# Kernel tuning notes

Hardware: AMD Instinct MI355X
Metric: run time of the kernel (lower is better)

## Reference

```python
import math
import jax, jax.numpy as jnp
import numpy as np

NUM_BUCKETS = 32
MAX_DISTANCE = 128
N_HEADS = 16
D_KV = 64


def _relative_position_bucket(relative_position, num_buckets=NUM_BUCKETS, max_distance=MAX_DISTANCE):
    # bidirectional (encoder) version, faithful to T5Attention._relative_position_bucket
    nb = num_buckets // 2
    rel_buckets = (relative_position > 0).astype(jnp.int32) * nb
    rp = jnp.abs(relative_position)
    max_exact = nb // 2
    is_small = rp < max_exact
    # log-spaced buckets for large distances; clamp arg of log to >=1 to avoid -inf
    rp_large = max_exact + (
        jnp.log(jnp.maximum(rp, 1).astype(jnp.float32) / max_exact)
        / math.log(max_distance / max_exact)
        * (nb - max_exact)
    ).astype(jnp.int32)
    rp_large = jnp.minimum(rp_large, nb - 1)
    return rel_buckets + jnp.where(is_small, rp, rp_large)


def setup_inputs() -> dict:
    key = jax.random.key(0)
    ks = jax.random.split(key, 6)
    B, S, D = 2, 2048, 1024
    scale = 0.02
    return {
        "hidden_states": jax.random.normal(ks[0], (B, S, D), dtype=jnp.float32),
        "Wq": jax.random.normal(ks[1], (D, N_HEADS * D_KV), dtype=jnp.float32) * scale,
        "Wk": jax.random.normal(ks[2], (D, N_HEADS * D_KV), dtype=jnp.float32) * scale,
        "Wv": jax.random.normal(ks[3], (D, N_HEADS * D_KV), dtype=jnp.float32) * scale,
        "Wo": jax.random.normal(ks[4], (N_HEADS * D_KV, D), dtype=jnp.float32) * scale,
        "rel_bias": jax.random.normal(ks[5], (NUM_BUCKETS, N_HEADS), dtype=jnp.float32),
    }


def reference(hidden_states, Wq, Wk, Wv, Wo, rel_bias):
    B, S, D = hidden_states.shape
    H, dk = N_HEADS, D_KV
    q = (hidden_states @ Wq).reshape(B, S, H, dk)
    k = (hidden_states @ Wk).reshape(B, S, H, dk)
    v = (hidden_states @ Wv).reshape(B, S, H, dk)

    pos = jnp.arange(S)
    relative_position = pos[None, :] - pos[:, None]          # [S_q, S_k]
    buckets = _relative_position_bucket(relative_position)    # [S_q, S_k]
    bias = rel_bias[buckets].transpose(2, 0, 1)               # [H, S_q, S_k]

    # T5 attention: NO 1/sqrt(d) scaling
    scores = jnp.einsum('bqhd,bkhd->bhqk', q, k) + bias[None]
    attn = jax.nn.softmax(scores, axis=-1)
    ctx = jnp.einsum('bhqk,bkhd->bqhd', attn, v).reshape(B, S, H * dk)
    return ctx @ Wo
```

## Files before the change

kernel.cpp:

```cpp
#include <hip/hip_runtime.h>
#include <stdint.h>

#define S_LEN 2048
#define NH 16
#define NB_DELTA (2*S_LEN-1)
#define FST 72

typedef __attribute__((ext_vector_type(8))) __bf16 bf16x8;
typedef __attribute__((ext_vector_type(4))) float f32x4;

__device__ __forceinline__ unsigned short f2bf(float f){
    union { float f; unsigned int u; } v; v.f = f;
    unsigned int u = v.u;
    return (unsigned short)((u + 0x7FFFu + ((u >> 16) & 1u)) >> 16);
}
__device__ __forceinline__ unsigned short f2bf_fast(float f){
    union { float f; unsigned int u; } v; v.f = f;
    return (unsigned short)((v.u + 0x8000u) >> 16);
}

__device__ __forceinline__ void gload16(const void* g, void* l){
    __builtin_amdgcn_global_load_lds(
        (const __attribute__((address_space(1))) void*)(uintptr_t)g,
        (__attribute__((address_space(3))) void*)(uintptr_t)l, 16, 0, 0);
}

__global__ __launch_bounds__(256) void cast_bias_kernel(const float* __restrict__ in,
                                                        unsigned short* __restrict__ out, int n,
                                                        const float* __restrict__ rel_bias,
                                                        float* __restrict__ biasT){
    int i = (blockIdx.x * blockDim.x + threadIdx.x) * 4;
    if (i < n) {
        float4 f = *(const float4*)(in + i);
        ushort4 o;
        o.x = f2bf(f.x); o.y = f2bf(f.y); o.z = f2bf(f.z); o.w = f2bf(f.w);
        *(ushort4*)(out + i) = o;
    }
    if (blockIdx.x < 16) {
        int t = blockIdx.x * 256 + threadIdx.x;
        if (t < NB_DELTA) {
            int delta = t - (S_LEN - 1);
            int bucket = (delta > 0) ? 16 : 0;
            int a = delta < 0 ? -delta : delta;
            int b;
            if (a < 8) b = a;
            else {
                int bl = 33 - __builtin_clz(a * a);
                b = bl < 15 ? bl : 15;
            }
            bucket += b;
            for (int h = 0; h < NH; h++)
                biasT[h * NB_DELTA + t] = rel_bias[bucket * NH + h];
        }
    }
}

__global__ __launch_bounds__(256) void transpose_cast4_kernel(
    const float* __restrict__ W0, const float* __restrict__ W1,
    const float* __restrict__ W2, const float* __restrict__ W3,
    unsigned short* __restrict__ D0, unsigned short* __restrict__ D1,
    unsigned short* __restrict__ D2, unsigned short* __restrict__ D3){
    const float* src; unsigned short* dst;
    switch (blockIdx.z) {
        case 0: src = W0; dst = D0; break;
        case 1: src = W1; dst = D1; break;
        case 2: src = W2; dst = D2; break;
        default: src = W3; dst = D3; break;
    }
    __shared__ float tile[32][33];
    int bx = blockIdx.x, by = blockIdx.y;
    int tx = threadIdx.x & 31, ty = threadIdx.x >> 5;
    for (int i = 0; i < 4; i++)
        tile[ty + 8*i][tx] = src[(size_t)(by*32 + ty + 8*i) * 1024 + bx*32 + tx];
    __syncthreads();
    for (int i = 0; i < 4; i++)
        dst[(size_t)(bx*32 + ty + 8*i) * 1024 + by*32 + tx] = f2bf(tile[tx][ty + 8*i]);
}

template<int MODE, int BM>
__global__ __launch_bounds__(256) void gemm_bt_kernel(const unsigned short* __restrict__ A,
                                                      const unsigned short* __restrict__ BT,
                                                      float* __restrict__ C0,
                                                      unsigned short* __restrict__ C1,
                                                      unsigned short* __restrict__ C2,
                                                      int Kdim, int ldc){
    constexpr int IT = BM / 32;
    __shared__ __align__(16) unsigned short As[BM * 32];
    __shared__ __align__(16) unsigned short Bs[128 * 32];
    const int t = threadIdx.x;
    const int wave = t >> 6, lane = t & 63;
    const int quad = lane >> 4, l16 = lane & 15;
    const int wm = (wave >> 1) * (BM / 2), wn = (wave & 1) * 64;
    const size_t row0 = (size_t)blockIdx.y * BM, col0 = (size_t)blockIdx.x * 128;

    const unsigned short* ga = A  + (row0 + wave * (BM/4) + (lane >> 2)) * (size_t)Kdim + (lane & 3) * 8;
    const unsigned short* gb = BT + (col0 + wave * 32 + (lane >> 2)) * (size_t)Kdim + (lane & 3) * 8;
    unsigned short* la0 = &As[(wave * (BM/4)) * 32];
    unsigned short* la1 = &As[(wave * (BM/4) + 16) * 32];
    unsigned short* lb0 = &Bs[(wave * 32) * 32];
    unsigned short* lb1 = &Bs[(wave * 32 + 16) * 32];
    const size_t rstep = (size_t)16 * Kdim;

    f32x4 acc[IT][4] = {};

    for (int kt = 0; kt < Kdim; kt += 32) {
        gload16(ga + kt, la0);
        if (BM == 128) gload16(ga + rstep + kt, la1);
        gload16(gb + kt,         lb0);
        gload16(gb + rstep + kt, lb1);
        __syncthreads();
        bf16x8 a[IT], b[4];
        for (int i = 0; i < IT; i++)
            a[i] = *(const bf16x8*)(&As[(wm + i*16 + l16) * 32 + quad * 8]);
        for (int j = 0; j < 4; j++)
            b[j] = *(const bf16x8*)(&Bs[(wn + j*16 + l16) * 32 + quad * 8]);
        for (int i = 0; i < IT; i++)
            for (int j = 0; j < 4; j++)
                acc[i][j] = __builtin_amdgcn_mfma_f32_16x16x32_bf16(a[i], b[j], acc[i][j], 0, 0, 0);
        __syncthreads();
    }
    for (int i = 0; i < IT; i++)
        for (int j = 0; j < 4; j++) {
            size_t r0 = row0 + wm + i*16 + quad*4;
            size_t c  = col0 + wn + j*16 + l16;
            if (MODE == 0) {
                for (int r = 0; r < 4; r++)
                    C0[(r0 + r) * ldc + c] = acc[i][j][r];
            } else {
                if (c < 2048) {
                    for (int r = 0; r < 4; r++)
                        C1[(r0 + r) * 2048 + c] = f2bf(acc[i][j][r]);
                } else {
                    int bb = (int)(r0 >> 11);
                    int s  = (int)(r0 & 2047);
                    ushort4 pk;
                    pk.x = f2bf(acc[i][j][0]); pk.y = f2bf(acc[i][j][1]);
                    pk.z = f2bf(acc[i][j][2]); pk.w = f2bf(acc[i][j][3]);
                    *(ushort4*)(C2 + ((size_t)(bb * 1024) + (c - 2048)) * 2048 + s) = pk;
                }
            }
        }
}

__global__ __launch_bounds__(256, 4) void flash5_kernel(
    const unsigned short* __restrict__ qk,
    const unsigned short* __restrict__ vt,
    const float* __restrict__ biasT,
    float* __restrict__ ctxp,
    float* __restrict__ rsbuf)
{
    const int qt = blockIdx.x, h = blockIdx.y;
    const int b = blockIdx.z >> 1, ck = blockIdx.z & 1;
    const int kt0 = ck << 10;
    const int t = threadIdx.x;
    const int w = t >> 6, lane = t & 63, quad = lane >> 4, l16 = lane & 15;
    const int q0 = qt * 128;

    __shared__ __align__(16) unsigned short smem[128 * FST];
    __shared__ __align__(16) unsigned short Pb[128 * FST];
    __shared__ float bias_s[192];
    unsigned short* Qs  = smem;
    unsigned short* Ks  = smem;
    unsigned short* Vts = smem + 64 * FST;

    for (int s = 0; s < 4; s++) {
        int g = t + s * 256;
        int r = g >> 3, c = (g & 7) * 8;
        *(int4*)&Qs[r * FST + c] =
            *(const int4*)(qk + (size_t)(b * S_LEN + q0 + r) * 2048 + h * 64 + c);
    }
    __syncthreads();
    bf16x8 qb[2][2];
    for (int nt = 0; nt < 2; nt++)
        for (int ks = 0; ks < 2; ks++)
            qb[ks][nt] = *(const bf16x8*)&Qs[(w * 32 + nt * 16 + l16) * FST + ks * 32 + quad * 8];

    float rsum[2] = {0.f, 0.f};
    f32x4 ctx[4][2] = {};

    const float* biasRow = biasT + h * NB_DELTA + 2047;

    for (int kt = kt0; kt < kt0 + 1024; kt += 64) {
        __syncthreads();
        {
            int r0 = t >> 3, c0 = (t & 7) * 8;
            int g1 = t + 256;
            int r1 = g1 >> 3, c1 = (g1 & 7) * 8;
            const unsigned short* kbase = qk + (size_t)(b * S_LEN + kt) * 2048 + 1024 + h * 64;
            *(int4*)&Ks[r0 * FST + c0] = *(const int4*)(kbase + (size_t)r0 * 2048 + c0);
            *(int4*)&Ks[r1 * FST + c1] = *(const int4*)(kbase + (size_t)r1 * 2048 + c1);
            const unsigned short* vbase = vt + (size_t)(b * 1024 + h * 64) * 2048 + kt;
            *(int4*)&Vts[r0 * FST + c0] = *(const int4*)(vbase + (size_t)r0 * 2048 + c0);
            *(int4*)&Vts[r1 * FST + c1] = *(const int4*)(vbase + (size_t)r1 * 2048 + c1);
            if (t < 192) bias_s[t] = biasRow[kt - q0 - 127 + t] - 16.0f;
        }
        __syncthreads();

        f32x4 st[4][2] = {};
        for (int ks = 0; ks < 2; ks++)
            for (int nb = 0; nb < 4; nb++) {
                bf16x8 ka = *(const bf16x8*)&Ks[(nb * 16 + l16) * FST + ks * 32 + quad * 8];
                st[nb][0] = __builtin_amdgcn_mfma_f32_16x16x32_bf16(ka, qb[ks][0], st[nb][0], 0, 0, 0);
                st[nb][1] = __builtin_amdgcn_mfma_f32_16x16x32_bf16(ka, qb[ks][1], st[nb][1], 0, 0, 0);
            }
        for (int nt = 0; nt < 2; nt++) {
            const int ib = quad * 4 + 127 - w * 32 - nt * 16 - l16;
            float rs = 0.f;
            for (int nb = 0; nb < 4; nb++) {
                float e0 = __expf(st[nb][nt][0] + bias_s[ib + nb * 16 + 0]);
                float e1 = __expf(st[nb][nt][1] + bias_s[ib + nb * 16 + 1]);
                float e2 = __expf(st[nb][nt][2] + bias_s[ib + nb * 16 + 2]);
                float e3 = __expf(st[nb][nt][3] + bias_s[ib + nb * 16 + 3]);
                rs += (e0 + e1) + (e2 + e3);
                ushort4 pk;
                pk.x = f2bf_fast(e0); pk.y = f2bf_fast(e1);
                pk.z = f2bf_fast(e2); pk.w = f2bf_fast(e3);
                *(ushort4*)&Pb[(w * 32 + nt * 16 + l16) * FST + nb * 16 + quad * 4] = pk;
            }
            rsum[nt] += rs;
        }
        for (int ks = 0; ks < 2; ks++) {
            bf16x8 pb0 = *(const bf16x8*)&Pb[(w * 32 + l16) * FST + ks * 32 + quad * 8];
            bf16x8 pb1 = *(const bf16x8*)&Pb[(w * 32 + 16 + l16) * FST + ks * 32 + quad * 8];
            for (int nd = 0; nd < 4; nd++) {
                bf16x8 va = *(const bf16x8*)&Vts[(nd * 16 + l16) * FST + ks * 32 + quad * 8];
                ctx[nd][0] = __builtin_amdgcn_mfma_f32_16x16x32_bf16(va, pb0, ctx[nd][0], 0, 0, 0);
                ctx[nd][1] = __builtin_amdgcn_mfma_f32_16x16x32_bf16(va, pb1, ctx[nd][1], 0, 0, 0);
            }
        }
    }
    float* cp = ctxp + (size_t)ck * 4096 * 1024;
    for (int nt = 0; nt < 2; nt++) {
        float rs = rsum[nt];
        rs += __shfl_xor(rs, 16, 64);
        rs += __shfl_xor(rs, 32, 64);
        int row = b * S_LEN + q0 + w * 32 + nt * 16 + l16;
        if (quad == 0) rsbuf[((size_t)ck * 4096 + row) * 16 + h] = rs;
        for (int nd = 0; nd < 4; nd++) {
            float4 pv;
            pv.x = ctx[nd][nt][0]; pv.y = ctx[nd][nt][1];
            pv.z = ctx[nd][nt][2]; pv.w = ctx[nd][nt][3];
            *(float4*)&cp[(size_t)row * 1024 + h * 64 + nd * 16 + quad * 4] = pv;
        }
    }
}

__global__ __launch_bounds__(256) void combine_kernel(const float* __restrict__ ctxp,
                                                      const float* __restrict__ rsbuf,
                                                      unsigned short* __restrict__ ctxb){
    int e = blockIdx.x * 256 + threadIdx.x;
    int row = e >> 8;
    int c4 = (e & 255) * 4;
    int h = c4 >> 6;
    float l = rsbuf[(size_t)row * 16 + h] + rsbuf[((size_t)4096 + row) * 16 + h];
    float4 a = *(const float4*)&ctxp[(size_t)row * 1024 + c4];
    float4 bb = *(const float4*)&ctxp[(size_t)4096 * 1024 + (size_t)row * 1024 + c4];
    float inv = 1.f / l;
    ushort4 o;
    o.x = f2bf((a.x + bb.x) * inv); o.y = f2bf((a.y + bb.y) * inv);
    o.z = f2bf((a.z + bb.z) * inv); o.w = f2bf((a.w + bb.w) * inv);
    *(ushort4*)&ctxb[(size_t)row * 1024 + c4] = o;
}

extern "C" void kernel_launch(void* const* d_in, const int* in_sizes, int n_in,
                              void* d_out, int out_size, void* d_ws, size_t ws_size,
                              hipStream_t stream) {
    const float* hs       = (const float*)d_in[0];
    const float* Wq       = (const float*)d_in[1];
    const float* Wk       = (const float*)d_in[2];
    const float* Wv       = (const float*)d_in[3];
    const float* Wo       = (const float*)d_in[4];
    const float* rel_bias = (const float*)d_in[5];
    float* out = (float*)d_out;

    char* ws = (char*)d_ws;
    float* biasT          = (float*)ws;           ws += 262144;
    unsigned short* hsb   = (unsigned short*)ws;  ws += 8388608;
    unsigned short* WT    = (unsigned short*)ws;  ws += 6291456;
    unsigned short* WoT   = (unsigned short*)ws;  ws += 2097152;
    unsigned short* qkbuf = (unsigned short*)ws;  ws += 16777216;
    unsigned short* Vtg   = (unsigned short*)ws;  ws += 8388608;
    unsigned short* ctxb  = (unsigned short*)ws;  ws += 8388608;
    float* ctxp           = (float*)ws;           ws += 33554432;
    float* rsbuf          = (float*)ws;

    cast_bias_kernel<<<4096, 256, 0, stream>>>(hs, hsb, 4194304, rel_bias, biasT);
    transpose_cast4_kernel<<<dim3(32, 32, 4), 256, 0, stream>>>(
        Wq, Wk, Wv, Wo, WT, WT + 1024 * 1024, WT + 2 * 1024 * 1024, WoT);

    gemm_bt_kernel<1, 128><<<dim3(24, 32), 256, 0, stream>>>(hsb, WT, nullptr, qkbuf, Vtg, 1024, 0);
    flash5_kernel<<<dim3(S_LEN / 128, NH, 4), 256, 0, stream>>>(qkbuf, Vtg, biasT, ctxp, rsbuf);
    combine_kernel<<<4096, 256, 0, stream>>>(ctxp, rsbuf, ctxb);
    gemm_bt_kernel<0, 64><<<dim3(8, 64), 256, 0, stream>>>(ctxb, WoT, out, nullptr, nullptr, 1024, 1024);
}
```

Baseline: 211.6 us.

## Merge prep kernels, use direct global-to-LDS loads, store bf16 partial context

Merges the hidden-state cast/bias kernel and the weight transpose kernel into one launch, removing one kernel launch. In the attention kernel, K/V tiles are now loaded with global_load_lds 16-byte direct copies into an unpadded split layout, bypassing registers. The per-split partial context is written as bf16 instead of fp32, halving that intermediate's write and read traffic in flash and combine. Risks are LDS bank conflicts from the unpadded 32-wide layout and extra rounding of unnormalised partial sums.

New measurement: 209.0 us. About the same (-1.3%).

```diff
diff --git a/kernel.cpp b/kernel.cpp
--- a/kernel.cpp
+++ b/kernel.cpp
@@ -4,7 +4,7 @@
 #define S_LEN 2048
 #define NH 16
 #define NB_DELTA (2*S_LEN-1)
-#define FST 72
+#define PST 72
 
 typedef __attribute__((ext_vector_type(8))) __bf16 bf16x8;
 typedef __attribute__((ext_vector_type(4))) float f32x4;
@@ -18,6 +18,10 @@
     union { float f; unsigned int u; } v; v.f = f;
     return (unsigned short)((v.u + 0x8000u) >> 16);
 }
+__device__ __forceinline__ float bf2f(unsigned short u){
+    union { unsigned int u; float f; } v; v.u = ((unsigned int)u) << 16;
+    return v.f;
+}
 
 __device__ __forceinline__ void gload16(const void* g, void* l){
     __builtin_amdgcn_global_load_lds(
@@ -25,41 +29,41 @@
         (__attribute__((address_space(3))) void*)(uintptr_t)l, 16, 0, 0);
 }
 
-__global__ __launch_bounds__(256) void cast_bias_kernel(const float* __restrict__ in,
-                                                        unsigned short* __restrict__ out, int n,
-                                                        const float* __restrict__ rel_bias,
-                                                        float* __restrict__ biasT){
-    int i = (blockIdx.x * blockDim.x + threadIdx.x) * 4;
-    if (i < n) {
-        float4 f = *(const float4*)(in + i);
-        ushort4 o;
-        o.x = f2bf(f.x); o.y = f2bf(f.y); o.z = f2bf(f.z); o.w = f2bf(f.w);
-        *(ushort4*)(out + i) = o;
-    }
-    if (blockIdx.x < 16) {
-        int t = blockIdx.x * 256 + threadIdx.x;
-        if (t < NB_DELTA) {
-            int delta = t - (S_LEN - 1);
-            int bucket = (delta > 0) ? 16 : 0;
-            int a = delta < 0 ? -delta : delta;
-            int b;
-            if (a < 8) b = a;
-            else {
-                int bl = 33 - __builtin_clz(a * a);
-                b = bl < 15 ? bl : 15;
-            }
-            bucket += b;
-            for (int h = 0; h < NH; h++)
-                biasT[h * NB_DELTA + t] = rel_bias[bucket * NH + h];
-        }
-    }
-}
-
-__global__ __launch_bounds__(256) void transpose_cast4_kernel(
+__global__ __launch_bounds__(256) void prep_kernel(
+    const float* __restrict__ hs, unsigned short* __restrict__ hsb,
     const float* __restrict__ W0, const float* __restrict__ W1,
     const float* __restrict__ W2, const float* __restrict__ W3,
     unsigned short* __restrict__ D0, unsigned short* __restrict__ D1,
-    unsigned short* __restrict__ D2, unsigned short* __restrict__ D3){
+    unsigned short* __restrict__ D2, unsigned short* __restrict__ D3,
+    const float* __restrict__ rel_bias, float* __restrict__ biasT){
+    if (blockIdx.z == 4) {
+        int bi = blockIdx.y * 32 + blockIdx.x;
+        for (int it = 0; it < 4; it++) {
+            int i = bi * 4096 + it * 1024 + threadIdx.x * 4;
+            float4 f = *(const float4*)(hs + i);
+            ushort4 o;
+            o.x = f2bf(f.x); o.y = f2bf(f.y); o.z = f2bf(f.z); o.w = f2bf(f.w);
+            *(ushort4*)(hsb + i) = o;
+        }
+        if (bi < 16) {
+            int t = bi * 256 + threadIdx.x;
+            if (t < NB_DELTA) {
+                int delta = t - (S_LEN - 1);
+                int bucket = (delta > 0) ? 16 : 0;
+                int a = delta < 0 ? -delta : delta;
+                int b;
+                if (a < 8) b = a;
+                else {
+                    int bl = 33 - __builtin_clz(a * a);
+                    b = bl < 15 ? bl : 15;
+                }
+                bucket += b;
+                for (int h = 0; h < NH; h++)
+                    biasT[h * NB_DELTA + t] = rel_bias[bucket * NH + h];
+            }
+        }
+        return;
+    }
     const float* src; unsigned short* dst;
     switch (blockIdx.z) {
         case 0: src = W0; dst = D0; break;
@@ -142,11 +146,11 @@
         }
 }
 
-__global__ __launch_bounds__(256, 4) void flash5_kernel(
+__global__ __launch_bounds__(256, 4) void flash6_kernel(
     const unsigned short* __restrict__ qk,
     const unsigned short* __restrict__ vt,
     const float* __restrict__ biasT,
-    float* __restrict__ ctxp,
+    unsigned short* __restrict__ ctxpb,
     float* __restrict__ rsbuf)
 {
     const int qt = blockIdx.x, h = blockIdx.y;
@@ -156,42 +160,43 @@
     const int w = t >> 6, lane = t & 63, quad = lane >> 4, l16 = lane & 15;
     const int q0 = qt * 128;
 
-    __shared__ __align__(16) unsigned short smem[128 * FST];
-    __shared__ __align__(16) unsigned short Pb[128 * FST];
+    __shared__ __align__(16) unsigned short KV[4][64 * 32];
+    __shared__ __align__(16) unsigned short Pb[128 * PST];
     __shared__ float bias_s[192];
-    unsigned short* Qs  = smem;
-    unsigned short* Ks  = smem;
-    unsigned short* Vts = smem + 64 * FST;
 
     for (int s = 0; s < 4; s++) {
         int g = t + s * 256;
         int r = g >> 3, c = (g & 7) * 8;
-        *(int4*)&Qs[r * FST + c] =
+        *(int4*)&Pb[r * PST + c] =
             *(const int4*)(qk + (size_t)(b * S_LEN + q0 + r) * 2048 + h * 64 + c);
     }
     __syncthreads();
     bf16x8 qb[2][2];
     for (int nt = 0; nt < 2; nt++)
         for (int ks = 0; ks < 2; ks++)
-            qb[ks][nt] = *(const bf16x8*)&Qs[(w * 32 + nt * 16 + l16) * FST + ks * 32 + quad * 8];
+            qb[ks][nt] = *(const bf16x8*)&Pb[(w * 32 + nt * 16 + l16) * PST + ks * 32 + quad * 8];
 
     float rsum[2] = {0.f, 0.f};
     f32x4 ctx[4][2] = {};
 
     const float* biasRow = biasT + h * NB_DELTA + 2047;
+
+    const int srow = w * 16 + (lane >> 2);
+    const int scol = (lane & 3) * 8;
+    unsigned short* ldsK0 = &KV[0][w * 16 * 32];
+    unsigned short* ldsK1 = &KV[1][w * 16 * 32];
+    unsigned short* ldsV0 = &KV[2][w * 16 * 32];
+    unsigned short* ldsV1 = &KV[3][w * 16 * 32];
 
     for (int kt = kt0; kt < kt0 + 1024; kt += 64) {
         __syncthreads();
         {
-            int r0 = t >> 3, c0 = (t & 7) * 8;
-            int g1 = t + 256;
-            int r1 = g1 >> 3, c1 = (g1 & 7) * 8;
-            const unsigned short* kbase = qk + (size_t)(b * S_LEN + kt) * 2048 + 1024 + h * 64;
-            *(int4*)&Ks[r0 * FST + c0] = *(const int4*)(kbase + (size_t)r0 * 2048 + c0);
-            *(int4*)&Ks[r1 * FST + c1] = *(const int4*)(kbase + (size_t)r1 * 2048 + c1);
-            const unsigned short* vbase = vt + (size_t)(b * 1024 + h * 64) * 2048 + kt;
-            *(int4*)&Vts[r0 * FST + c0] = *(const int4*)(vbase + (size_t)r0 * 2048 + c0);
-            *(int4*)&Vts[r1 * FST + c1] = *(const int4*)(vbase + (size_t)r1 * 2048 + c1);
+            const unsigned short* kb = qk + (size_t)(b * S_LEN + kt + srow) * 2048 + 1024 + h * 64 + scol;
+            const unsigned short* vb = vt + (size_t)(b * 1024 + h * 64 + srow) * 2048 + kt + scol;
+            gload16(kb,      ldsK0);
+            gload16(kb + 32, ldsK1);
+            gload16(vb,      ldsV0);
+            gload16(vb + 32, ldsV1);
             if (t < 192) bias_s[t] = biasRow[kt - q0 - 127 + t] - 16.0f;
         }
         __syncthreads();
@@ -199,7 +204,7 @@
         f32x4 st[4][2] = {};
         for (int ks = 0; ks < 2; ks++)
             for (int nb = 0; nb < 4; nb++) {
-                bf16x8 ka = *(const bf16x8*)&Ks[(nb * 16 + l16) * FST + ks * 32 + quad * 8];
+                bf16x8 ka = *(const bf16x8*)&KV[ks][(nb * 16 + l16) * 32 + quad * 8];
                 st[nb][0] = __builtin_amdgcn_mfma_f32_16x16x32_bf16(ka, qb[ks][0], st[nb][0], 0, 0, 0);
                 st[nb][1] = __builtin_amdgcn_mfma_f32_16x16x32_bf16(ka, qb[ks][1], st[nb][1], 0, 0, 0);
             }
@@ -215,21 +220,21 @@
                 ushort4 pk;
                 pk.x = f2bf_fast(e0); pk.y = f2bf_fast(e1);
                 pk.z = f2bf_fast(e2); pk.w = f2bf_fast(e3);
-                *(ushort4*)&Pb[(w * 32 + nt * 16 + l16) * FST + nb * 16 + quad * 4] = pk;
+                *(ushort4*)&Pb[(w * 32 + nt * 16 + l16) * PST + nb * 16 + quad * 4] = pk;
             }
             rsum[nt] += rs;
         }
         for (int ks = 0; ks < 2; ks++) {
-            bf16x8 pb0 = *(const bf16x8*)&Pb[(w * 32 + l16) * FST + ks * 32 + quad * 8];
-            bf16x8 pb1 = *(const bf16x8*)&Pb[(w * 32 + 16 + l16) * FST + ks * 32 + quad * 8];
+            bf16x8 pb0 = *(const bf16x8*)&Pb[(w * 32 + l16) * PST + ks * 32 + quad * 8];
+            bf16x8 pb1 = *(const bf16x8*)&Pb[(w * 32 + 16 + l16) * PST + ks * 32 + quad * 8];
             for (int nd = 0; nd < 4; nd++) {
-                bf16x8 va = *(const bf16x8*)&Vts[(nd * 16 + l16) * FST + ks * 32 + quad * 8];
+                bf16x8 va = *(const bf16x8*)&KV[2 + ks][(nd * 16 + l16) * 32 + quad * 8];
                 ctx[nd][0] = __builtin_amdgcn_mfma_f32_16x16x32_bf16(va, pb0, ctx[nd][0], 0, 0, 0);
                 ctx[nd][1] = __builtin_amdgcn_mfma_f32_16x16x32_bf16(va, pb1, ctx[nd][1], 0, 0, 0);
             }
         }
     }
-    float* cp = ctxp + (size_t)ck * 4096 * 1024;
+    unsigned short* cp = ctxpb + (size_t)ck * 4096 * 1024;
     for (int nt = 0; nt < 2; nt++) {
         float rs = rsum[nt];
         rs += __shfl_xor(rs, 16, 64);
@@ -237,15 +242,15 @@
         int row = b * S_LEN + q0 + w * 32 + nt * 16 + l16;
         if (quad == 0) rsbuf[((size_t)ck * 4096 + row) * 16 + h] = rs;
         for (int nd = 0; nd < 4; nd++) {
-            float4 pv;
-            pv.x = ctx[nd][nt][0]; pv.y = ctx[nd][nt][1];
-            pv.z = ctx[nd][nt][2]; pv.w = ctx[nd][nt][3];
-            *(float4*)&cp[(size_t)row * 1024 + h * 64 + nd * 16 + quad * 4] = pv;
-        }
-    }
-}
-
-__global__ __launch_bounds__(256) void combine_kernel(const float* __restrict__ ctxp,
+            ushort4 pk;
+            pk.x = f2bf(ctx[nd][nt][0]); pk.y = f2bf(ctx[nd][nt][1]);
+            pk.z = f2bf(ctx[nd][nt][2]); pk.w = f2bf(ctx[nd][nt][3]);
+            *(ushort4*)&cp[(size_t)row * 1024 + h * 64 + nd * 16 + quad * 4] = pk;
+        }
+    }
+}
+
+__global__ __launch_bounds__(256) void combine_kernel(const unsigned short* __restrict__ ctxpb,
                                                       const float* __restrict__ rsbuf,
                                                       unsigned short* __restrict__ ctxb){
     int e = blockIdx.x * 256 + threadIdx.x;
@@ -253,12 +258,14 @@
     int c4 = (e & 255) * 4;
     int h = c4 >> 6;
     float l = rsbuf[(size_t)row * 16 + h] + rsbuf[((size_t)4096 + row) * 16 + h];
-    float4 a = *(const float4*)&ctxp[(size_t)row * 1024 + c4];
-    float4 bb = *(const float4*)&ctxp[(size_t)4096 * 1024 + (size_t)row * 1024 + c4];
+    ushort4 a  = *(const ushort4*)&ctxpb[(size_t)row * 1024 + c4];
+    ushort4 b2 = *(const ushort4*)&ctxpb[(size_t)4096 * 1024 + (size_t)row * 1024 + c4];
     float inv = 1.f / l;
     ushort4 o;
-    o.x = f2bf((a.x + bb.x) * inv); o.y = f2bf((a.y + bb.y) * inv);
-    o.z = f2bf((a.z + bb.z) * inv); o.w = f2bf((a.w + bb.w) * inv);
+    o.x = f2bf((bf2f(a.x) + bf2f(b2.x)) * inv);
+    o.y = f2bf((bf2f(a.y) + bf2f(b2.y)) * inv);
+    o.z = f2bf((bf2f(a.z) + bf2f(b2.z)) * inv);
+    o.w = f2bf((bf2f(a.w) + bf2f(b2.w)) * inv);
     *(ushort4*)&ctxb[(size_t)row * 1024 + c4] = o;
 }
 
@@ -281,15 +288,15 @@
     unsigned short* qkbuf = (unsigned short*)ws;  ws += 16777216;
     unsigned short* Vtg   = (unsigned short*)ws;  ws += 8388608;
     unsigned short* ctxb  = (unsigned short*)ws;  ws += 8388608;
-    float* ctxp           = (float*)ws;           ws += 33554432;
+    unsigned short* ctxpb = (unsigned short*)ws;  ws += 16777216;
     float* rsbuf          = (float*)ws;
 
-    cast_bias_kernel<<<4096, 256, 0, stream>>>(hs, hsb, 4194304, rel_bias, biasT);
-    transpose_cast4_kernel<<<dim3(32, 32, 4), 256, 0, stream>>>(
-        Wq, Wk, Wv, Wo, WT, WT + 1024 * 1024, WT + 2 * 1024 * 1024, WoT);
+    prep_kernel<<<dim3(32, 32, 5), 256, 0, stream>>>(
+        hs, hsb, Wq, Wk, Wv, Wo,
+        WT, WT + 1024 * 1024, WT + 2 * 1024 * 1024, WoT, rel_bias, biasT);
 
     gemm_bt_kernel<1, 128><<<dim3(24, 32), 256, 0, stream>>>(hsb, WT, nullptr, qkbuf, Vtg, 1024, 0);
-    flash5_kernel<<<dim3(S_LEN / 128, NH, 4), 256, 0, stream>>>(qkbuf, Vtg, biasT, ctxp, rsbuf);
-    combine_kernel<<<4096, 256, 0, stream>>>(ctxp, rsbuf, ctxb);
+    flash6_kernel<<<dim3(S_LEN / 128, NH, 4), 256, 0, stream>>>(qkbuf, Vtg, biasT, ctxpb, rsbuf);
+    combine_kernel<<<4096, 256, 0, stream>>>(ctxpb, rsbuf, ctxb);
     gemm_bt_kernel<0, 64><<<dim3(8, 64), 256, 0, stream>>>(ctxb, WoT, out, nullptr, nullptr, 1024, 1024);
 }
```
